# Optimization experiments

Measured on AMD Instinct MI355X. Metric: run time of the kernel, lower is better.

The kernel has to match this reference:

```python
import jax, jax.numpy as jnp
import numpy as np

N = 100000      # nodes
E = 1600000     # edges
D_IN = 128
D_H = 128
D_OUT = 128


def setup_inputs() -> dict:
    key = jax.random.key(0)
    ks = jax.random.split(key, 8)
    x = jax.random.normal(ks[0], (N, D_IN), dtype=jnp.float32)
    edge_index = jax.random.randint(ks[1], (2, E), 0, N, dtype=jnp.int32)
    s = 1.0 / np.sqrt(D_IN)
    W1 = jax.random.uniform(ks[2], (D_IN, D_H), jnp.float32, -s, s)
    b1 = jnp.zeros((D_H,), jnp.float32)
    W2 = jax.random.uniform(ks[3], (D_H, D_H), jnp.float32, -s, s)
    b2 = jnp.zeros((D_H,), jnp.float32)
    W3 = jax.random.uniform(ks[4], (D_H, D_OUT), jnp.float32, -s, s)
    b3 = jnp.zeros((D_OUT,), jnp.float32)
    return {"x": x, "edge_index": edge_index,
            "W1": W1, "b1": b1, "W2": W2, "b2": b2, "W3": W3, "b3": b3}


def _gcn_conv(x, W, b, src, dst, norm, n_nodes):
    # PyG GCNConv: out = scatter_add(norm * (x @ W)[src] -> dst) + b
    h = x @ W
    msg = h[src] * norm[:, None]                       # [E+N, d]
    agg = jax.ops.segment_sum(msg, dst, num_segments=n_nodes)
    return agg + b


def reference(x, edge_index, W1, b1, W2, b2, W3, b3):
    n = x.shape[0]
    loop = jnp.arange(n, dtype=edge_index.dtype)
    src = jnp.concatenate([edge_index[0], loop])       # add self-loops
    dst = jnp.concatenate([edge_index[1], loop])
    # symmetric normalization: deg computed on target (incl. self-loops)
    deg = jax.ops.segment_sum(jnp.ones_like(dst, dtype=x.dtype), dst,
                              num_segments=n)
    dis = jnp.where(deg > 0, jax.lax.rsqrt(jnp.maximum(deg, 1.0)), 0.0)
    norm = dis[src] * dis[dst]                         # [E+N]

    h = _gcn_conv(x, W1, b1, src, dst, norm, n)
    h = jax.nn.relu(h)                                 # dropout: eval mode = identity
    h = _gcn_conv(h, W2, b2, src, dst, norm, n)
    h = jax.nn.relu(h)
    out = _gcn_conv(h, W3, b3, src, dst, norm, n)
    return out
```

## Files before the change

kernel.cpp:

```cpp
#include <hip/hip_runtime.h>
#include <hip/hip_fp16.h>

#define D 128
#define NPB 256
#define KMAX 512
#define CHUNK 4096

typedef _Float16 half_t;
typedef _Float16 f16x8 __attribute__((ext_vector_type(8)));
typedef float f32x4 __attribute__((ext_vector_type(4)));


__global__ __launch_bounds__(256) void zero_int(int* __restrict__ p, int n) {
    int i = blockIdx.x * 256 + threadIdx.x;
    if (i < n) p[i] = 0;
}

__global__ __launch_bounds__(256) void bucket_hist_kernel(const int* __restrict__ dst,
                                                          int* __restrict__ bucket_cnt, int E) {
    __shared__ int scnt[KMAX];
    int t = threadIdx.x;
    for (int i = t; i < KMAX; i += 256) scnt[i] = 0;
    __syncthreads();
    int base = blockIdx.x * CHUNK;
    int nE = min(CHUNK, E - base);
    for (int i = t; i < nE; i += 256)
        atomicAdd(&scnt[dst[base + i] >> 8], 1);
    __syncthreads();
    for (int i = t; i < KMAX; i += 256)
        if (scnt[i]) atomicAdd(&bucket_cnt[i], scnt[i]);
}

__global__ __launch_bounds__(KMAX) void bucket_scan_kernel(const int* __restrict__ bucket_cnt,
                                                           int* __restrict__ bucket_ptr,
                                                           int* __restrict__ bucket_cur,
                                                           int K, int E) {
    __shared__ int sh[KMAX];
    int t = threadIdx.x;
    int v = (t < K) ? bucket_cnt[t] : 0;
    sh[t] = v;
    __syncthreads();
    for (int off = 1; off < KMAX; off <<= 1) {
        int add = (t >= off) ? sh[t - off] : 0;
        __syncthreads();
        sh[t] += add;
        __syncthreads();
    }
    if (t < K) {
        int ex = sh[t] - v;
        bucket_ptr[t] = ex;
        bucket_cur[t] = ex;
    }
    if (t == 0) bucket_ptr[K] = E;
}

__global__ __launch_bounds__(256) void bucket_scatter_kernel(const int* __restrict__ src,
                                                             const int* __restrict__ dst,
                                                             int* __restrict__ bucket_cur,
                                                             int2* __restrict__ bdata, int E) {
    __shared__ int sdst[CHUNK];
    __shared__ int scnt[KMAX];
    __shared__ int sbase[KMAX];
    int t = threadIdx.x;
    int base = blockIdx.x * CHUNK;
    int nE = min(CHUNK, E - base);
    for (int i = t; i < KMAX; i += 256) scnt[i] = 0;
    __syncthreads();
    for (int i = t; i < nE; i += 256) {
        int d = dst[base + i];
        sdst[i] = d;
        atomicAdd(&scnt[d >> 8], 1);
    }
    __syncthreads();
    for (int i = t; i < KMAX; i += 256) {
        int c = scnt[i];
        sbase[i] = c ? atomicAdd(&bucket_cur[i], c) : 0;
        scnt[i] = 0;
    }
    __syncthreads();
    for (int i = t; i < nE; i += 256) {
        int d = sdst[i];
        int b = d >> 8;
        int pos = sbase[b] + atomicAdd(&scnt[b], 1);
        bdata[pos] = make_int2(src[base + i], d);
    }
}

__global__ __launch_bounds__(256) void csr_count_scan_kernel(const int2* __restrict__ bdata,
                                                             const int* __restrict__ bucket_ptr,
                                                             int* __restrict__ row_ptr,
                                                             float* __restrict__ dis,
                                                             int n, int E, int K) {
    __shared__ int scnt[NPB];
    __shared__ int sh[NPB];
    int b = blockIdx.x;
    int node0 = b << 8;
    int nn = min(NPB, n - node0);
    int t = threadIdx.x;
    scnt[t] = 0;
    __syncthreads();
    int p0 = bucket_ptr[b], p1 = bucket_ptr[b + 1];
    for (int i = p0 + t; i < p1; i += 256)
        atomicAdd(&scnt[bdata[i].y - node0], 1);
    __syncthreads();
    int v = scnt[t];
    sh[t] = v;
    __syncthreads();
    for (int off = 1; off < NPB; off <<= 1) {
        int add = (t >= off) ? sh[t - off] : 0;
        __syncthreads();
        sh[t] += add;
        __syncthreads();
    }
    if (t < nn) {
        row_ptr[node0 + t] = p0 + sh[t] - v;
        dis[node0 + t] = rsqrtf((float)(v + 1));
    }
    if (b == K - 1 && t == 0) row_ptr[n] = E;
}

__global__ __launch_bounds__(256) void csr_fill_kernel(const int2* __restrict__ bdata,
                                                       const int* __restrict__ bucket_ptr,
                                                       const int* __restrict__ row_ptr,
                                                       int* __restrict__ csr_src, int n) {
    __shared__ int cursor[NPB];
    int b = blockIdx.x;
    int node0 = b << 8;
    int nn = min(NPB, n - node0);
    int t = threadIdx.x;
    if (t < nn) cursor[t] = row_ptr[node0 + t];
    __syncthreads();
    int p0 = bucket_ptr[b], p1 = bucket_ptr[b + 1];
    for (int i = p0 + t; i < p1; i += 256) {
        int2 e = bdata[i];
        int pos = atomicAdd(&cursor[e.y - node0], 1);
        csr_src[pos] = e.x;
    }
}


__global__ __launch_bounds__(256) void pack_w_kernel(const float* __restrict__ W,
                                                     half_t* __restrict__ Wf) {
    int b = blockIdx.x;
    int s = b >> 3, t = b & 7;
    int tid = threadIdx.x;
    for (int e = tid; e < 512; e += 256) {
        int l = e >> 3, j = e & 7;
        int k = s * 32 + ((l >> 4) & 3) * 4 + (j & 3) + ((j >> 2) << 4);
        int n = t * 16 + (l & 15);
        Wf[(size_t)((s * 8 + t) * 64 + l) * 8 + j] = (half_t)W[k * 128 + n];
    }
}


template <bool RELU>
__global__ __launch_bounds__(256) void gemm_mfma_kernel(const float* __restrict__ A,
                                                        const half_t* __restrict__ Wf,
                                                        const float* __restrict__ dis,
                                                        half_t* __restrict__ C, int n) {
    __shared__ half_t sA[64 * 132];
    int tid = threadIdx.x;
    int base = blockIdx.x * 64;

    const float4* A4 = (const float4*)A;
#pragma unroll
    for (int it = 0; it < 8; ++it) {
        int idx = it * 256 + tid;
        int r = idx >> 5, kq = idx & 31;
        int grow = base + r;
        float4 va = (grow < n) ? A4[(size_t)grow * 32 + kq]
                               : make_float4(0.f, 0.f, 0.f, 0.f);
        if (RELU) {
            va.x = fmaxf(va.x, 0.f); va.y = fmaxf(va.y, 0.f);
            va.z = fmaxf(va.z, 0.f); va.w = fmaxf(va.w, 0.f);
        }
        union { half_t h[4]; float2 f2; } pk;
        pk.h[0] = (half_t)va.x; pk.h[1] = (half_t)va.y;
        pk.h[2] = (half_t)va.z; pk.h[3] = (half_t)va.w;
        *(float2*)&sA[r * 132 + kq * 4] = pk.f2;
    }
    __syncthreads();

    int l = tid & 63, w = tid >> 6;
    int m = l & 15, g = l >> 4;
    int R = w * 16;

    f32x4 acc[8];
#pragma unroll
    for (int t = 0; t < 8; ++t) acc[t] = (f32x4){0.f, 0.f, 0.f, 0.f};

    const f16x8* WF = (const f16x8*)Wf;
#pragma unroll
    for (int s = 0; s < 4; ++s) {
        union { f16x8 v; float2 f2[2]; } af;
        int a_off = (R + m) * 132 + s * 32 + 4 * g;
        af.f2[0] = *(const float2*)&sA[a_off];
        af.f2[1] = *(const float2*)&sA[a_off + 16];
#pragma unroll
        for (int t = 0; t < 8; ++t) {
            f16x8 bf = WF[(size_t)(s * 8 + t) * 64 + l];
            acc[t] = __builtin_amdgcn_mfma_f32_16x16x32_f16(af.v, bf, acc[t], 0, 0, 0);
        }
    }

    int row0 = base + R + 4 * g;
    float dd[4];
#pragma unroll
    for (int r = 0; r < 4; ++r) dd[r] = (row0 + r < n) ? dis[row0 + r] : 0.f;
#pragma unroll
    for (int t = 0; t < 8; ++t) {
        int col = t * 16 + m;
#pragma unroll
        for (int r = 0; r < 4; ++r) {
            int row = row0 + r;
            if (row < n) C[(size_t)row * D + col] = (half_t)(acc[t][r] * dd[r]);
        }
    }
}


__global__ __launch_bounds__(256) void aggregate_kernel(const __half2* __restrict__ Hs,
                                                        const int* __restrict__ row_ptr,
                                                        const int* __restrict__ csr_src,
                                                        const float* __restrict__ dis,
                                                        const float* __restrict__ b,
                                                        float* __restrict__ out, int n) {
    int node = blockIdx.x * 4 + (threadIdx.x >> 6);
    if (node >= n) return;
    int lane = threadIdx.x & 63;

    float2 s0 = __half22float2(Hs[(size_t)node * 64 + lane]);
    float accx = s0.x, accy = s0.y;

    int p0 = row_ptr[node], p1 = row_ptr[node + 1];
    int p = p0;
    int nb8 = (p1 - p0) >> 3;
    if (nb8 > 0) {
        int idx[8];
#pragma unroll
        for (int u = 0; u < 8; ++u) idx[u] = csr_src[p + u];
        for (int bb = 1; bb < nb8; ++bb) {
            int nxt[8];
#pragma unroll
            for (int u = 0; u < 8; ++u) nxt[u] = csr_src[p + 8 + u];
            __half2 v[8];
#pragma unroll
            for (int u = 0; u < 8; ++u) v[u] = Hs[(size_t)idx[u] * 64 + lane];
#pragma unroll
            for (int u = 0; u < 8; ++u) {
                float2 f = __half22float2(v[u]);
                accx += f.x; accy += f.y;
            }
#pragma unroll
            for (int u = 0; u < 8; ++u) idx[u] = nxt[u];
            p += 8;
        }
        {
            __half2 v[8];
#pragma unroll
            for (int u = 0; u < 8; ++u) v[u] = Hs[(size_t)idx[u] * 64 + lane];
#pragma unroll
            for (int u = 0; u < 8; ++u) {
                float2 f = __half22float2(v[u]);
                accx += f.x; accy += f.y;
            }
            p += 8;
        }
    }
    for (; p + 4 <= p1; p += 4) {
        int s0i = csr_src[p + 0];
        int s1i = csr_src[p + 1];
        int s2i = csr_src[p + 2];
        int s3i = csr_src[p + 3];
        __half2 v0 = Hs[(size_t)s0i * 64 + lane];
        __half2 v1 = Hs[(size_t)s1i * 64 + lane];
        __half2 v2 = Hs[(size_t)s2i * 64 + lane];
        __half2 v3 = Hs[(size_t)s3i * 64 + lane];
        float2 f0 = __half22float2(v0), f1 = __half22float2(v1);
        float2 f2 = __half22float2(v2), f3 = __half22float2(v3);
        accx += f0.x; accy += f0.y;
        accx += f1.x; accy += f1.y;
        accx += f2.x; accy += f2.y;
        accx += f3.x; accy += f3.y;
    }
    for (; p < p1; ++p) {
        int s = csr_src[p];
        float2 f = __half22float2(Hs[(size_t)s * 64 + lane]);
        accx += f.x; accy += f.y;
    }

    float di = dis[node];
    float2 bb2 = *(const float2*)(b + 2 * lane);
    float2 o;
    o.x = fmaf(accx, di, bb2.x);
    o.y = fmaf(accy, di, bb2.y);
    ((float2*)(out + (size_t)node * D))[lane] = o;
}


extern "C" void kernel_launch(void* const* d_in, const int* in_sizes, int n_in,
                              void* d_out, int out_size, void* d_ws, size_t ws_size,
                              hipStream_t stream) {
    const float* x  = (const float*)d_in[0];
    const int*   ei = (const int*)d_in[1];
    const float* W1 = (const float*)d_in[2];
    const float* b1 = (const float*)d_in[3];
    const float* W2 = (const float*)d_in[4];
    const float* b2 = (const float*)d_in[5];
    const float* W3 = (const float*)d_in[6];
    const float* b3 = (const float*)d_in[7];
    float* out = (float*)d_out;

    int n = in_sizes[0] / D;
    int E = in_sizes[1] / 2;
    const int* src = ei;
    const int* dst = ei + E;
    int K = (n + NPB - 1) >> 8;

    char* ws = (char*)d_ws;
    half_t* hbuf     = (half_t*)ws; ws += (size_t)n * D * sizeof(float);
    float* dis       = (float*)ws;  ws += (size_t)n * sizeof(float);
    int* row_ptr     = (int*)ws;    ws += (size_t)(n + 1) * sizeof(int);
    int* csr_src     = (int*)ws;    ws += (size_t)E * sizeof(int);
    int* bucket_cnt  = (int*)ws;    ws += KMAX * sizeof(int);
    int* bucket_ptr  = (int*)ws;    ws += (KMAX + 1) * sizeof(int);
    int* bucket_cur  = (int*)ws;    ws += KMAX * sizeof(int);
    int2* bdata      = (int2*)hbuf;
    half_t* Wf1      = hbuf + (size_t)n * D;
    half_t* Wf2      = Wf1 + 128 * 128;
    half_t* Wf3      = Wf2 + 128 * 128;

    int gC = (E + CHUNK - 1) / CHUNK;
    int gM = (n + 63) / 64;
    int gA = (n + 3) / 4;

    pack_w_kernel<<<32, 256, 0, stream>>>(W1, Wf1);
    pack_w_kernel<<<32, 256, 0, stream>>>(W2, Wf2);
    pack_w_kernel<<<32, 256, 0, stream>>>(W3, Wf3);

    zero_int<<<2, 256, 0, stream>>>(bucket_cnt, KMAX);
    bucket_hist_kernel<<<gC, 256, 0, stream>>>(dst, bucket_cnt, E);
    bucket_scan_kernel<<<1, KMAX, 0, stream>>>(bucket_cnt, bucket_ptr, bucket_cur, K, E);
    bucket_scatter_kernel<<<gC, 256, 0, stream>>>(src, dst, bucket_cur, bdata, E);
    csr_count_scan_kernel<<<K, 256, 0, stream>>>(bdata, bucket_ptr, row_ptr, dis, n, E, K);
    csr_fill_kernel<<<K, 256, 0, stream>>>(bdata, bucket_ptr, row_ptr, csr_src, n);

    gemm_mfma_kernel<false><<<gM, 256, 0, stream>>>(x, Wf1, dis, hbuf, n);
    aggregate_kernel<<<gA, 256, 0, stream>>>((const __half2*)hbuf, row_ptr, csr_src, dis, b1, out, n);
    gemm_mfma_kernel<true><<<gM, 256, 0, stream>>>(out, Wf2, dis, hbuf, n);
    aggregate_kernel<<<gA, 256, 0, stream>>>((const __half2*)hbuf, row_ptr, csr_src, dis, b2, out, n);
    gemm_mfma_kernel<true><<<gM, 256, 0, stream>>>(out, Wf3, dis, hbuf, n);
    aggregate_kernel<<<gA, 256, 0, stream>>>((const __half2*)hbuf, row_ptr, csr_src, dis, b3, out, n);
}
```

Measured before the change: 455.9 us.

## Store intermediate activations in fp16 with fused ReLU and coalesced GEMM stores

The first two aggregation kernels now apply ReLU and write their outputs as fp16 into a separate buffer, so the following GEMMs read half the bytes and skip the fp32-to-fp16 conversion. The GEMM epilogue stages results through padded LDS and writes 16-byte coalesced rows instead of scattered 2-byte stores. The workspace is reorganised so the packed weights live in their own region. This trades an extra fp16 rounding of hidden activations for lower memory traffic between layers.

```diff
diff --git a/kernel.cpp b/kernel.cpp
--- a/kernel.cpp
+++ b/kernel.cpp
@@ -2,6 +2,7 @@
 #include <hip/hip_fp16.h>
 
 #define D 128
+#define TPAD 136
 #define NPB 256
 #define KMAX 512
 #define CHUNK 4096
@@ -153,12 +154,58 @@
 }
 
 
-template <bool RELU>
-__global__ __launch_bounds__(256) void gemm_mfma_kernel(const float* __restrict__ A,
-                                                        const half_t* __restrict__ Wf,
-                                                        const float* __restrict__ dis,
-                                                        half_t* __restrict__ C, int n) {
-    __shared__ half_t sA[64 * 132];
+__device__ __forceinline__ void gemm_core_epilogue(half_t* sA, int tid, int base,
+                                                   const float* __restrict__ dis,
+                                                   half_t* __restrict__ C, int n,
+                                                   f32x4 acc[8], int l, int w) {
+    int m = l & 15, g = l >> 4;
+    int R = w * 16;
+    int row0 = base + R + 4 * g;
+    float dd[4];
+#pragma unroll
+    for (int r = 0; r < 4; ++r) dd[r] = (row0 + r < n) ? dis[row0 + r] : 0.f;
+    __syncthreads();
+#pragma unroll
+    for (int t = 0; t < 8; ++t) {
+#pragma unroll
+        for (int r = 0; r < 4; ++r)
+            sA[(R + 4 * g + r) * TPAD + t * 16 + m] = (half_t)(acc[t][r] * dd[r]);
+    }
+    __syncthreads();
+#pragma unroll
+    for (int q = 0; q < 4; ++q) {
+        int f4 = q * 256 + tid;
+        int r = f4 >> 4, c = f4 & 15;
+        int row = base + r;
+        if (row < n)
+            *(float4*)&C[(size_t)row * D + c * 8] = *(const float4*)&sA[r * TPAD + c * 8];
+    }
+}
+
+__device__ __forceinline__ void gemm_mfma_loop(const half_t* sA, const half_t* __restrict__ Wf,
+                                               f32x4 acc[8], int l, int w) {
+    int m = l & 15, g = l >> 4;
+    int R = w * 16;
+    const f16x8* WF = (const f16x8*)Wf;
+#pragma unroll
+    for (int s = 0; s < 4; ++s) {
+        union { f16x8 v; float2 f2[2]; } af;
+        int a_off = (R + m) * TPAD + s * 32 + 4 * g;
+        af.f2[0] = *(const float2*)&sA[a_off];
+        af.f2[1] = *(const float2*)&sA[a_off + 16];
+#pragma unroll
+        for (int t = 0; t < 8; ++t) {
+            f16x8 bf = WF[(size_t)(s * 8 + t) * 64 + l];
+            acc[t] = __builtin_amdgcn_mfma_f32_16x16x32_f16(af.v, bf, acc[t], 0, 0, 0);
+        }
+    }
+}
+
+__global__ __launch_bounds__(256) void gemm_mfma_f32in(const float* __restrict__ A,
+                                                       const half_t* __restrict__ Wf,
+                                                       const float* __restrict__ dis,
+                                                       half_t* __restrict__ C, int n) {
+    __shared__ half_t sA[64 * TPAD];
     int tid = threadIdx.x;
     int base = blockIdx.x * 64;
 
@@ -170,61 +217,57 @@
         int grow = base + r;
         float4 va = (grow < n) ? A4[(size_t)grow * 32 + kq]
                                : make_float4(0.f, 0.f, 0.f, 0.f);
-        if (RELU) {
-            va.x = fmaxf(va.x, 0.f); va.y = fmaxf(va.y, 0.f);
-            va.z = fmaxf(va.z, 0.f); va.w = fmaxf(va.w, 0.f);
-        }
         union { half_t h[4]; float2 f2; } pk;
         pk.h[0] = (half_t)va.x; pk.h[1] = (half_t)va.y;
         pk.h[2] = (half_t)va.z; pk.h[3] = (half_t)va.w;
-        *(float2*)&sA[r * 132 + kq * 4] = pk.f2;
+        *(float2*)&sA[r * TPAD + kq * 4] = pk.f2;
     }
     __syncthreads();
 
     int l = tid & 63, w = tid >> 6;
-    int m = l & 15, g = l >> 4;
-    int R = w * 16;
-
     f32x4 acc[8];
 #pragma unroll
     for (int t = 0; t < 8; ++t) acc[t] = (f32x4){0.f, 0.f, 0.f, 0.f};
-
-    const f16x8* WF = (const f16x8*)Wf;
-#pragma unroll
-    for (int s = 0; s < 4; ++s) {
-        union { f16x8 v; float2 f2[2]; } af;
-        int a_off = (R + m) * 132 + s * 32 + 4 * g;
-        af.f2[0] = *(const float2*)&sA[a_off];
-        af.f2[1] = *(const float2*)&sA[a_off + 16];
-#pragma unroll
-        for (int t = 0; t < 8; ++t) {
-            f16x8 bf = WF[(size_t)(s * 8 + t) * 64 + l];
-            acc[t] = __builtin_amdgcn_mfma_f32_16x16x32_f16(af.v, bf, acc[t], 0, 0, 0);
-        }
-    }
-
-    int row0 = base + R + 4 * g;
-    float dd[4];
-#pragma unroll
-    for (int r = 0; r < 4; ++r) dd[r] = (row0 + r < n) ? dis[row0 + r] : 0.f;
-#pragma unroll
-    for (int t = 0; t < 8; ++t) {
-        int col = t * 16 + m;
-#pragma unroll
-        for (int r = 0; r < 4; ++r) {
-            int row = row0 + r;
-            if (row < n) C[(size_t)row * D + col] = (half_t)(acc[t][r] * dd[r]);
-        }
-    }
-}
-
-
+    gemm_mfma_loop(sA, Wf, acc, l, w);
+    gemm_core_epilogue(sA, tid, base, dis, C, n, acc, l, w);
+}
+
+__global__ __launch_bounds__(256) void gemm_mfma_f16in(const half_t* __restrict__ A,
+                                                       const half_t* __restrict__ Wf,
+                                                       const float* __restrict__ dis,
+                                                       half_t* __restrict__ C, int n) {
+    __shared__ half_t sA[64 * TPAD];
+    int tid = threadIdx.x;
+    int base = blockIdx.x * 64;
+
+    const float4* A4 = (const float4*)A;
+#pragma unroll
+    for (int it = 0; it < 4; ++it) {
+        int idx = it * 256 + tid;
+        int r = idx >> 4, c16 = idx & 15;
+        int grow = base + r;
+        float4 va = (grow < n) ? A4[(size_t)grow * 16 + c16]
+                               : make_float4(0.f, 0.f, 0.f, 0.f);
+        *(float4*)&sA[r * TPAD + c16 * 8] = va;
+    }
+    __syncthreads();
+
+    int l = tid & 63, w = tid >> 6;
+    f32x4 acc[8];
+#pragma unroll
+    for (int t = 0; t < 8; ++t) acc[t] = (f32x4){0.f, 0.f, 0.f, 0.f};
+    gemm_mfma_loop(sA, Wf, acc, l, w);
+    gemm_core_epilogue(sA, tid, base, dis, C, n, acc, l, w);
+}
+
+
+template <bool F16OUT>
 __global__ __launch_bounds__(256) void aggregate_kernel(const __half2* __restrict__ Hs,
                                                         const int* __restrict__ row_ptr,
                                                         const int* __restrict__ csr_src,
                                                         const float* __restrict__ dis,
                                                         const float* __restrict__ b,
-                                                        float* __restrict__ out, int n) {
+                                                        void* __restrict__ outv, int n) {
     int node = blockIdx.x * 4 + (threadIdx.x >> 6);
     if (node >= n) return;
     int lane = threadIdx.x & 63;
@@ -291,10 +334,16 @@
 
     float di = dis[node];
     float2 bb2 = *(const float2*)(b + 2 * lane);
-    float2 o;
-    o.x = fmaf(accx, di, bb2.x);
-    o.y = fmaf(accy, di, bb2.y);
-    ((float2*)(out + (size_t)node * D))[lane] = o;
+    float ox = fmaf(accx, di, bb2.x);
+    float oy = fmaf(accy, di, bb2.y);
+    if (F16OUT) {
+        ox = fmaxf(ox, 0.f);
+        oy = fmaxf(oy, 0.f);
+        ((__half2*)outv)[(size_t)node * 64 + lane] = __floats2half2_rn(ox, oy);
+    } else {
+        float2 o; o.x = ox; o.y = oy;
+        ((float2*)((float*)outv + (size_t)node * D))[lane] = o;
+    }
 }
 
 
@@ -318,17 +367,18 @@
     int K = (n + NPB - 1) >> 8;
 
     char* ws = (char*)d_ws;
-    half_t* hbuf     = (half_t*)ws; ws += (size_t)n * D * sizeof(float);
+    half_t* hbuf     = (half_t*)ws; ws += (size_t)n * D * sizeof(half_t);
+    half_t* outh     = (half_t*)ws; ws += (size_t)n * D * sizeof(half_t);
     float* dis       = (float*)ws;  ws += (size_t)n * sizeof(float);
     int* row_ptr     = (int*)ws;    ws += (size_t)(n + 1) * sizeof(int);
     int* csr_src     = (int*)ws;    ws += (size_t)E * sizeof(int);
     int* bucket_cnt  = (int*)ws;    ws += KMAX * sizeof(int);
     int* bucket_ptr  = (int*)ws;    ws += (KMAX + 1) * sizeof(int);
     int* bucket_cur  = (int*)ws;    ws += KMAX * sizeof(int);
+    half_t* Wf1      = (half_t*)ws; ws += 128 * 128 * sizeof(half_t);
+    half_t* Wf2      = (half_t*)ws; ws += 128 * 128 * sizeof(half_t);
+    half_t* Wf3      = (half_t*)ws; ws += 128 * 128 * sizeof(half_t);
     int2* bdata      = (int2*)hbuf;
-    half_t* Wf1      = hbuf + (size_t)n * D;
-    half_t* Wf2      = Wf1 + 128 * 128;
-    half_t* Wf3      = Wf2 + 128 * 128;
 
     int gC = (E + CHUNK - 1) / CHUNK;
     int gM = (n + 63) / 64;
@@ -345,10 +395,10 @@
     csr_count_scan_kernel<<<K, 256, 0, stream>>>(bdata, bucket_ptr, row_ptr, dis, n, E, K);
     csr_fill_kernel<<<K, 256, 0, stream>>>(bdata, bucket_ptr, row_ptr, csr_src, n);
 
-    gemm_mfma_kernel<false><<<gM, 256, 0, stream>>>(x, Wf1, dis, hbuf, n);
-    aggregate_kernel<<<gA, 256, 0, stream>>>((const __half2*)hbuf, row_ptr, csr_src, dis, b1, out, n);
-    gemm_mfma_kernel<true><<<gM, 256, 0, stream>>>(out, Wf2, dis, hbuf, n);
-    aggregate_kernel<<<gA, 256, 0, stream>>>((const __half2*)hbuf, row_ptr, csr_src, dis, b2, out, n);
-    gemm_mfma_kernel<true><<<gM, 256, 0, stream>>>(out, Wf3, dis, hbuf, n);
-    aggregate_kernel<<<gA, 256, 0, stream>>>((const __half2*)hbuf, row_ptr, csr_src, dis, b3, out, n);
-}
+    gemm_mfma_f32in<<<gM, 256, 0, stream>>>(x, Wf1, dis, hbuf, n);
+    aggregate_kernel<true><<<gA, 256, 0, stream>>>((const __half2*)hbuf, row_ptr, csr_src, dis, b1, outh, n);
+    gemm_mfma_f16in<<<gM, 256, 0, stream>>>(outh, Wf2, dis, hbuf, n);
+    aggregate_kernel<true><<<gA, 256, 0, stream>>>((const __half2*)hbuf, row_ptr, csr_src, dis, b2, outh, n);
+    gemm_mfma_f16in<<<gM, 256, 0, stream>>>(outh, Wf3, dis, hbuf, n);
+    aggregate_kernel<false><<<gA, 256, 0, stream>>>((const __half2*)hbuf, row_ptr, csr_src, dis, b3, out, n);
+}
```

Result: faster. 421.9 us (-7.4%).
